# Optimization experiments

Measured on AMD Instinct MI355X. Metric: run time of the kernel, lower is better.

The kernel has to match this reference:

```python
import jax, jax.numpy as jnp
import numpy as np

D = 1024      # hidden_dim
H = 16        # num_heads
KV = 8        # num_kv_heads
HD = D // H   # head_size = 64
M = 3584      # intermediate_dim
E = 8         # num_local_experts
TOPK = 2      # num_experts_per_tok
EPS = 1e-6
ROPE_THETA = 10000.0


def setup_inputs() -> dict:
    key = jax.random.key(0)
    ks = jax.random.split(key, 12)
    s = 0.02
    B, S = 2, 1024
    return {
        "x": jax.random.normal(ks[0], (B, S, D), jnp.float32),
        "ln1_w": jnp.ones((D,), jnp.float32),
        "ln2_w": jnp.ones((D,), jnp.float32),
        "wq": jax.random.normal(ks[1], (D, H * HD), jnp.float32) * s,
        "wk": jax.random.normal(ks[2], (D, KV * HD), jnp.float32) * s,
        "wv": jax.random.normal(ks[3], (D, KV * HD), jnp.float32) * s,
        "wo": jax.random.normal(ks[4], (H * HD, D), jnp.float32) * s,
        "router_w": jax.random.normal(ks[5], (D, E), jnp.float32) * s,
        "w_gate": jax.random.normal(ks[6], (E, D, M), jnp.float32) * s,
        "w_up": jax.random.normal(ks[7], (E, D, M), jnp.float32) * s,
        "w_down": jax.random.normal(ks[8], (E, M, D), jnp.float32) * s,
    }


def _rmsnorm(x, w, eps=EPS):
    xf = x.astype(jnp.float32)
    var = jnp.mean(xf * xf, axis=-1, keepdims=True)
    return (xf * jax.lax.rsqrt(var + eps)).astype(x.dtype) * w


def _rope(q, k):
    # q: [B,S,H,HD], k: [B,S,KV,HD]
    S = q.shape[1]
    inv_freq = 1.0 / (ROPE_THETA ** (jnp.arange(0, HD, 2, dtype=jnp.float32) / HD))
    ang = jnp.arange(S, dtype=jnp.float32)[:, None] * inv_freq[None, :]  # [S, HD/2]
    cos = jnp.concatenate([jnp.cos(ang), jnp.cos(ang)], axis=-1)[None, :, None, :]
    sin = jnp.concatenate([jnp.sin(ang), jnp.sin(ang)], axis=-1)[None, :, None, :]

    def rot_half(t):
        t1, t2 = jnp.split(t, 2, axis=-1)
        return jnp.concatenate([-t2, t1], axis=-1)

    return q * cos + rot_half(q) * sin, k * cos + rot_half(k) * sin


def reference(x, ln1_w, ln2_w, wq, wk, wv, wo, router_w, w_gate, w_up, w_down):
    B, S, _ = x.shape

    # ---- self-attention block ----
    h = _rmsnorm(x, ln1_w)
    q = (h @ wq).reshape(B, S, H, HD)
    k = (h @ wk).reshape(B, S, KV, HD)
    v = (h @ wv).reshape(B, S, KV, HD)
    q, k = _rope(q, k)
    rep = H // KV
    k = jnp.repeat(k, rep, axis=2)  # [B,S,H,HD]
    v = jnp.repeat(v, rep, axis=2)
    scores = jnp.einsum("bqhd,bkhd->bhqk", q, k) / jnp.sqrt(jnp.float32(HD))
    causal = jnp.tril(jnp.ones((S, S), bool))
    scores = jnp.where(causal[None, None], scores, jnp.finfo(scores.dtype).min)
    attn = jax.nn.softmax(scores, axis=-1)
    ao = jnp.einsum("bhqk,bkhd->bqhd", attn, v).reshape(B, S, H * HD)
    x = x + ao @ wo

    # ---- sparse MoE block (top-2 routing, SwiGLU experts) ----
    h = _rmsnorm(x, ln2_w)
    logits = h @ router_w                       # [B,S,E]
    probs = jax.nn.softmax(logits, axis=-1)
    topv, topi = jax.lax.top_k(probs, TOPK)     # [B,S,K]
    topv = topv / jnp.sum(topv, axis=-1, keepdims=True)
    # dense combine weights [B,S,E]: zero for unselected experts
    weights = jnp.sum(jax.nn.one_hot(topi, E, dtype=h.dtype) * topv[..., None], axis=-2)
    gate = jnp.einsum("bsd,edm->bsem", h, w_gate)
    up = jnp.einsum("bsd,edm->bsem", h, w_up)
    act = jax.nn.silu(gate) * up * weights[..., None]
    moe = jnp.einsum("bsem,emd->bsd", act, w_down)
    return x + moe
```

## Files before the change

kernel.cpp:

```cpp
#include <hip/hip_runtime.h>

typedef __attribute__((ext_vector_type(8))) short short8;
typedef __attribute__((ext_vector_type(4))) float f32x4;
typedef unsigned int u32;

#define DI static __device__ __forceinline__

DI unsigned short f2bf(float f) {
  unsigned u = __builtin_bit_cast(unsigned, f);
  u += 0x7fffu + ((u >> 16) & 1u);
  return (unsigned short)(u >> 16);
}
DI float bf2f(unsigned short b) {
  unsigned u = ((unsigned)b) << 16;
  return __builtin_bit_cast(float, u);
}

DI void gload16(const unsigned short* g, unsigned short* l) {
  __builtin_amdgcn_global_load_lds(
      (const __attribute__((address_space(1))) u32*)g,
      (__attribute__((address_space(3))) u32*)l, 16, 0, 0);
}

static constexpr int NT   = 2048;
static constexpr int SEQ  = 1024;
static constexpr int DIM  = 1024;
static constexpr int NH   = 16;
static constexpr int NKV  = 8;
static constexpr int HD   = 64;
static constexpr int MDIM = 3584;
static constexpr int NE   = 8;
static constexpr int QW   = 2048;
static constexpr int GUW  = 2 * MDIM;

__global__ void __launch_bounds__(256) transpose_kernel(
    const float* __restrict__ in, unsigned short* __restrict__ out,
    int R, int C, size_t in_estride, size_t out_estride) {
  __shared__ unsigned short tl[64][66];
  int e = blockIdx.z;
  const float* ip = in + (size_t)e * in_estride;
  unsigned short* op = out + (size_t)e * out_estride;
  int c0 = blockIdx.x * 64, r0 = blockIdx.y * 64;
  int tid = threadIdx.x;
  {
    int lr = tid >> 4, lc = (tid & 15) * 4;
#pragma unroll
    for (int p = 0; p < 4; ++p) {
      int r = p * 16 + lr;
      float4 v = *(const float4*)(ip + (size_t)(r0 + r) * C + c0 + lc);
      tl[lc + 0][r] = f2bf(v.x);
      tl[lc + 1][r] = f2bf(v.y);
      tl[lc + 2][r] = f2bf(v.z);
      tl[lc + 3][r] = f2bf(v.w);
    }
  }
  __syncthreads();
  {
    int c = tid >> 2, rc = (tid & 3) * 16;
    unsigned short tmp[16];
#pragma unroll
    for (int j = 0; j < 8; ++j) {
      u32 w = *(const u32*)&tl[c][rc + j * 2];
      tmp[j * 2] = (unsigned short)w;
      tmp[j * 2 + 1] = (unsigned short)(w >> 16);
    }
    unsigned short* dst = op + (size_t)(c0 + c) * R + r0 + rc;
#pragma unroll
    for (int j = 0; j < 2; ++j)
      *(uint4*)(dst + j * 8) = *(const uint4*)&tmp[j * 8];
  }
}

__global__ void __launch_bounds__(256) rmsnorm_kernel(const float* __restrict__ x,
                                                      const float* __restrict__ w,
                                                      unsigned short* __restrict__ out) {
  int row = blockIdx.x;
  const float* xr = x + (size_t)row * DIM;
  int i = threadIdx.x * 4;
  float4 v = *(const float4*)(xr + i);
  float s = v.x * v.x + v.y * v.y + v.z * v.z + v.w * v.w;
  for (int o = 32; o; o >>= 1) s += __shfl_xor(s, o);
  __shared__ float red[4];
  if ((threadIdx.x & 63) == 0) red[threadIdx.x >> 6] = s;
  __syncthreads();
  s = red[0] + red[1] + red[2] + red[3];
  float r = rsqrtf(s * (1.0f / DIM) + 1e-6f);
  float4 wv = *(const float4*)(w + i);
  ushort4 o4;
  o4.x = f2bf(v.x * r * wv.x);
  o4.y = f2bf(v.y * r * wv.y);
  o4.z = f2bf(v.z * r * wv.z);
  o4.w = f2bf(v.w * r * wv.w);
  *(ushort4*)(out + (size_t)row * DIM + i) = o4;
}

template <int GATHER, int EPI, int NNT>
__global__ void __launch_bounds__(256) gemmT_kernel(
    const unsigned short* __restrict__ A, int lda,
    const unsigned short* __restrict__ B, int ldb, size_t b_estride,
    void* __restrict__ Cv, int ldc,
    const float* __restrict__ resid,
    int M, int K,
    const int* __restrict__ lists, const int* __restrict__ cnt,
    int ks_count, size_t ks_stride) {
  constexpr int BN = NNT * 32;
  constexpr int NBLK = BN / 64;
  int zz = blockIdx.z;
  int e = zz / ks_count, ks = zz - e * ks_count;
  int KL = K / ks_count;
  int kbase = ks * KL;

  int count = M;
  const int* lst = nullptr;
  if (GATHER != 0) {
    count = cnt[e];
    if (count <= 0) return;
    lst = lists + e * NT;
    B += b_estride * (size_t)e;
  }
  int m0 = blockIdx.y * 128;
  if (m0 >= count) return;
  int n0 = blockIdx.x * BN;

  __shared__ unsigned short sA[3][128 * 32];
  __shared__ unsigned short sB[3][BN * 32];

  int tid = threadIdx.x, w = tid >> 6, lane = tid & 63;
  int l15 = lane & 15, lhi = lane >> 4;

  int srow = w * 16 + (lane >> 2);
  int schunk = ((lane & 3) ^ ((lane >> 2) & 3)) * 8;
  const unsigned short *aSrc0, *aSrc1;
  const unsigned short* bSrc[NBLK];
  {
    int mr0 = m0 + srow, mr1 = m0 + 64 + srow;
    int ar0, ar1;
    if (GATHER == 0) { ar0 = mr0; ar1 = mr1; }
    else {
      int c0i = mr0 < count ? mr0 : count - 1;
      int c1i = mr1 < count ? mr1 : count - 1;
      int p0 = lst[c0i], p1 = lst[c1i];
      ar0 = (GATHER == 1) ? (p0 >> 1) : p0;
      ar1 = (GATHER == 1) ? (p1 >> 1) : p1;
    }
    aSrc0 = A + (size_t)ar0 * lda + kbase + schunk;
    aSrc1 = A + (size_t)ar1 * lda + kbase + schunk;
#pragma unroll
    for (int s = 0; s < NBLK; ++s)
      bSrc[s] = B + (size_t)(n0 + s * 64 + srow) * ldb + kbase + schunk;
  }
  unsigned ldst = (unsigned)(w * 16) * 32;

  auto stage = [&](int buf, int k0) {
    gload16(aSrc0 + k0, &sA[buf][ldst]);
    gload16(aSrc1 + k0, &sA[buf][ldst + 64 * 32]);
#pragma unroll
    for (int s = 0; s < NBLK; ++s)
      gload16(bSrc[s] + k0, &sB[buf][ldst + s * 64 * 32]);
  };

  f32x4 acc[4][NNT] = {};
  int wm = w >> 1, wn = w & 1;
  int aoff[4], boff[NNT];
#pragma unroll
  for (int t = 0; t < 4; ++t) {
    int row = wm * 64 + t * 16 + l15;
    aoff[t] = row * 32 + ((lhi ^ (row & 3)) * 8);
  }
#pragma unroll
  for (int t = 0; t < NNT; ++t) {
    int col = wn * (BN / 2) + t * 16 + l15;
    boff[t] = col * 32 + ((lhi ^ (col & 3)) * 8);
  }

  int nsteps = KL / 32;
  stage(0, 0);
  if (nsteps > 1) stage(1, 32);

  int cur = 0, stg = 2;
  for (int t = 0; t < nsteps; ++t) {
    if (t + 1 < nsteps) {
      if constexpr (NNT == 8) asm volatile("s_waitcnt vmcnt(6)" ::: "memory");
      else                    asm volatile("s_waitcnt vmcnt(4)" ::: "memory");
    } else {
      asm volatile("s_waitcnt vmcnt(0)" ::: "memory");
    }
    __builtin_amdgcn_s_barrier();
    __builtin_amdgcn_sched_barrier(0);
    if (t + 2 < nsteps) stage(stg, (t + 2) * 32);
    const unsigned short* pa = sA[cur];
    const unsigned short* pb = sB[cur];
    short8 af[4], bfr[NNT];
#pragma unroll
    for (int q = 0; q < 4; ++q) af[q] = *(const short8*)&pa[aoff[q]];
#pragma unroll
    for (int q = 0; q < NNT; ++q) bfr[q] = *(const short8*)&pb[boff[q]];
    __builtin_amdgcn_s_setprio(1);
#pragma unroll
    for (int mi = 0; mi < 4; ++mi)
#pragma unroll
      for (int ni = 0; ni < NNT; ++ni)
        acc[mi][ni] =
            __builtin_amdgcn_mfma_f32_16x16x32_bf16(af[mi], bfr[ni], acc[mi][ni], 0, 0, 0);
    __builtin_amdgcn_s_setprio(0);
    cur = (cur == 2) ? 0 : cur + 1;
    stg = (stg == 2) ? 0 : stg + 1;
  }

#pragma unroll
  for (int mi = 0; mi < 4; ++mi) {
#pragma unroll
    for (int r = 0; r < 4; ++r) {
      int mr = m0 + wm * 64 + mi * 16 + lhi * 4 + r;
      if (GATHER != 0 && mr >= count) continue;
      size_t crow = (GATHER != 0) ? (size_t)lst[mr] : (size_t)mr;
#pragma unroll
      for (int ni = 0; ni < NNT; ++ni) {
        int n = n0 + wn * (BN / 2) + ni * 16 + l15;
        float val = acc[mi][ni][r];
        if (EPI == 0)
          ((unsigned short*)Cv)[crow * ldc + n] = f2bf(val);
        else if (EPI == 1)
          ((float*)Cv)[crow * ldc + n] = val + resid[crow * ldc + n];
        else
          ((float*)Cv)[(size_t)ks * ks_stride + crow * ldc + n] = val;
      }
    }
  }
}

__global__ void __launch_bounds__(256) rope_kernel(unsigned short* __restrict__ qkv) {
  int g = blockIdx.x * 256 + threadIdx.x;
  int i = g & 31;
  int hh = (g >> 5) % (NH + NKV);
  int tok = g / (32 * (NH + NKV));
  if (tok >= NT) return;
  int s = tok & (SEQ - 1);
  float inv = exp2f((float)i * (-13.287712379549449f / 32.0f));
  float ang = (float)s * inv;
  float sn = sinf(ang);
  float c = cosf(ang);
  int col = (hh < NH) ? hh * HD : DIM + (hh - NH) * HD;
  unsigned short* ptr = qkv + (size_t)tok * QW + col;
  float a = bf2f(ptr[i]), b2 = bf2f(ptr[i + 32]);
  ptr[i] = f2bf(a * c - b2 * sn);
  ptr[i + 32] = f2bf(b2 * c + a * sn);
}

__global__ void __launch_bounds__(64) attn_kernel(const unsigned short* __restrict__ qkv,
                                                  unsigned short* __restrict__ ao) {
  __shared__ unsigned short Ps[16 * 64];
  int bid = blockIdx.x;
  int qt = bid & 63;
  int h = (bid >> 6) & 15;
  int b = bid >> 10;
  int lane = threadIdx.x, l15 = lane & 15, lhi = lane >> 4;
  int q0 = qt * 16, kvh = h >> 1;
  int kcol = DIM + kvh * HD, vcol = DIM + NKV * HD + kvh * HD;

  const unsigned short* qp = qkv + ((size_t)(b * SEQ + q0 + l15)) * QW + h * HD + lhi * 8;
  short8 aq0 = *(const short8*)qp;
  short8 aq1 = *(const short8*)(qp + 32);

  float m[4] = {-1e30f, -1e30f, -1e30f, -1e30f};
  float l[4] = {0.f, 0.f, 0.f, 0.f};
  f32x4 accO[4] = {};

  int nkb = (qt >> 2) + 1;
  for (int kb_ = 0; kb_ < nkb; ++kb_) {
    int kbase = kb_ * 64;
    f32x4 s[4];
#pragma unroll
    for (int ct = 0; ct < 4; ++ct) {
      const unsigned short* kp =
          qkv + ((size_t)(b * SEQ + kbase + ct * 16 + l15)) * QW + kcol + lhi * 8;
      short8 k0v = *(const short8*)kp;
      short8 k1v = *(const short8*)(kp + 32);
      f32x4 a = {};
      a = __builtin_amdgcn_mfma_f32_16x16x32_bf16(aq0, k0v, a, 0, 0, 0);
      a = __builtin_amdgcn_mfma_f32_16x16x32_bf16(aq1, k1v, a, 0, 0, 0);
      int kpos = kbase + ct * 16 + l15;
#pragma unroll
      for (int r = 0; r < 4; ++r) {
        float v = a[r] * 0.125f;
        if (kpos > q0 + lhi * 4 + r) v = -1e30f;
        s[ct][r] = v;
      }
    }
    float nm[4], al[4], rs[4];
#pragma unroll
    for (int r = 0; r < 4; ++r) {
      float mb = fmaxf(fmaxf(s[0][r], s[1][r]), fmaxf(s[2][r], s[3][r]));
      mb = fmaxf(mb, __shfl_xor(mb, 1));
      mb = fmaxf(mb, __shfl_xor(mb, 2));
      mb = fmaxf(mb, __shfl_xor(mb, 4));
      mb = fmaxf(mb, __shfl_xor(mb, 8));
      nm[r] = fmaxf(m[r], mb);
      al[r] = __expf(m[r] - nm[r]);
      m[r] = nm[r];
      rs[r] = 0.f;
    }
#pragma unroll
    for (int ct = 0; ct < 4; ++ct) {
#pragma unroll
      for (int r = 0; r < 4; ++r) {
        float p = __expf(s[ct][r] - nm[r]);
        rs[r] += p;
        int q = lhi * 4 + r;
        Ps[q * 64 + ((ct * 16 + l15) ^ (lhi << 4))] = f2bf(p);
      }
    }
#pragma unroll
    for (int r = 0; r < 4; ++r) {
      rs[r] += __shfl_xor(rs[r], 1);
      rs[r] += __shfl_xor(rs[r], 2);
      rs[r] += __shfl_xor(rs[r], 4);
      rs[r] += __shfl_xor(rs[r], 8);
      l[r] = l[r] * al[r] + rs[r];
    }
#pragma unroll
    for (int dt = 0; dt < 4; ++dt)
#pragma unroll
      for (int r = 0; r < 4; ++r) accO[dt][r] *= al[r];

    int pswz = (l15 >> 2) << 4;
    short8 ap0 = *(const short8*)&Ps[l15 * 64 + ((lhi * 8) ^ pswz)];
    short8 ap1 = *(const short8*)&Ps[l15 * 64 + ((32 + lhi * 8) ^ pswz)];
#pragma unroll
    for (int dt = 0; dt < 4; ++dt) {
#pragma unroll
      for (int ks = 0; ks < 2; ++ks) {
        const unsigned short* vp =
            qkv + ((size_t)(b * SEQ + kbase + ks * 32 + lhi * 8)) * QW + vcol + dt * 16 + l15;
        short8 vf;
#pragma unroll
        for (int j = 0; j < 8; ++j) vf[j] = (short)vp[(size_t)j * QW];
        accO[dt] = __builtin_amdgcn_mfma_f32_16x16x32_bf16(ks ? ap1 : ap0, vf, accO[dt], 0, 0, 0);
      }
    }
  }
  float invl[4];
#pragma unroll
  for (int r = 0; r < 4; ++r) invl[r] = 1.f / l[r];
#pragma unroll
  for (int dt = 0; dt < 4; ++dt)
#pragma unroll
    for (int r = 0; r < 4; ++r)
      ao[((size_t)(b * SEQ + q0 + lhi * 4 + r)) * DIM + h * HD + dt * 16 + l15] =
          f2bf(accO[dt][r] * invl[r]);
}

__global__ void zero_cnt_kernel(int* __restrict__ cnt) {
  if (threadIdx.x < NE) cnt[threadIdx.x] = 0;
}

__global__ void __launch_bounds__(64) router_kernel(const float* __restrict__ x2,
                                                    const float* __restrict__ ln2w,
                                                    const float* __restrict__ rw,
                                                    float* __restrict__ wts,
                                                    int* __restrict__ cnt,
                                                    int* __restrict__ lists) {
  int t = blockIdx.x, lane = threadIdx.x;
  const float* xr = x2 + (size_t)t * DIM;
  float xs[16];
  double ssq = 0.0;
#pragma unroll
  for (int j = 0; j < 16; ++j) {
    xs[j] = xr[lane + j * 64];
    ssq += (double)xs[j] * xs[j];
  }
  for (int o = 32; o; o >>= 1) ssq += __shfl_xor(ssq, o);
  double r = rsqrt(ssq * (1.0 / DIM) + 1e-6);
  double p[NE] = {};
#pragma unroll
  for (int j = 0; j < 16; ++j) {
    int i = lane + j * 64;
    double hv = (double)xs[j] * r * (double)ln2w[i];
    const float* rwp = rw + (size_t)i * NE;
#pragma unroll
    for (int e = 0; e < NE; ++e) p[e] += hv * (double)rwp[e];
  }
  for (int o = 32; o; o >>= 1) {
#pragma unroll
    for (int e = 0; e < NE; ++e) p[e] += __shfl_xor(p[e], o);
  }
  if (lane == 0) {
    int i1 = 0;
    for (int e = 1; e < NE; ++e)
      if (p[e] > p[i1]) i1 = e;
    int i2 = (i1 == 0) ? 1 : 0;
    for (int e = 0; e < NE; ++e)
      if (e != i1 && p[e] > p[i2]) i2 = e;
    double mx = fmax(p[i1], p[i2]);
    double e1 = exp(p[i1] - mx), e2 = exp(p[i2] - mx);
    double inv = 1.0 / (e1 + e2);
    wts[t * 2] = (float)(e1 * inv);
    wts[t * 2 + 1] = (float)(e2 * inv);
    int pos1 = atomicAdd(&cnt[i1], 1);
    lists[i1 * NT + pos1] = t * 2;
    int pos2 = atomicAdd(&cnt[i2], 1);
    lists[i2 * NT + pos2] = t * 2 + 1;
  }
}

__global__ void __launch_bounds__(256) swiglu_kernel(const unsigned short* __restrict__ gu,
                                                     const float* __restrict__ wts,
                                                     unsigned short* __restrict__ act) {
  size_t i = ((size_t)blockIdx.x * 256 + threadIdx.x) * 8;
  int pid = (int)(i / MDIM);
  int mcol = (int)(i - (size_t)pid * MDIM);
  float w = wts[pid];
  const unsigned short* row = gu + (size_t)pid * GUW;
  short8 g8 = *(const short8*)(row + mcol);
  short8 u8 = *(const short8*)(row + MDIM + mcol);
  short8 o8;
#pragma unroll
  for (int j = 0; j < 8; ++j) {
    float gv = bf2f((unsigned short)g8[j]);
    float uv = bf2f((unsigned short)u8[j]);
    float sv = gv / (1.f + __expf(-gv));
    o8[j] = (short)f2bf(sv * uv * w);
  }
  *(short8*)(act + i) = o8;
}

__global__ void __launch_bounds__(256) combine_kernel(const float* __restrict__ x2,
                                                      const float* __restrict__ part,
                                                      float* __restrict__ out) {
  const size_t KSS = (size_t)2 * NT * DIM;
  size_t idx = ((size_t)blockIdx.x * 256 + threadIdx.x) * 4;
  size_t t = idx >> 10;
  size_t d = idx & 1023;
  float4 a = *(const float4*)(x2 + idx);
  float4 b0 = *(const float4*)(part + (t * 2) * DIM + d);
  float4 c0 = *(const float4*)(part + (t * 2 + 1) * DIM + d);
  float4 b1 = *(const float4*)(part + KSS + (t * 2) * DIM + d);
  float4 c1 = *(const float4*)(part + KSS + (t * 2 + 1) * DIM + d);
  float4 o;
  o.x = a.x + b0.x + c0.x + b1.x + c1.x;
  o.y = a.y + b0.y + c0.y + b1.y + c1.y;
  o.z = a.z + b0.z + c0.z + b1.z + c1.z;
  o.w = a.w + b0.w + c0.w + b1.w + c1.w;
  *(float4*)(out + idx) = o;
}

extern "C" void kernel_launch(void* const* d_in, const int* in_sizes, int n_in,
                              void* d_out, int out_size, void* d_ws, size_t ws_size,
                              hipStream_t stream) {
  const float* x   = (const float*)d_in[0];
  const float* ln1 = (const float*)d_in[1];
  const float* ln2 = (const float*)d_in[2];
  const float* wq  = (const float*)d_in[3];
  const float* wk  = (const float*)d_in[4];
  const float* wv  = (const float*)d_in[5];
  const float* wo  = (const float*)d_in[6];
  const float* rw  = (const float*)d_in[7];
  const float* wg  = (const float*)d_in[8];
  const float* wu  = (const float*)d_in[9];
  const float* wd  = (const float*)d_in[10];
  float* out = (float*)d_out;

  char* p = (char*)d_ws;
  auto take = [&](size_t bytes) {
    char* q = p;
    p += (bytes + 255) & ~(size_t)255;
    return q;
  };
  unsigned short* wguT = (unsigned short*)take((size_t)NE * GUW * DIM * 2);
  unsigned short* wdT  = (unsigned short*)take((size_t)NE * DIM * MDIM * 2);
  float*          x2   = (float*)take((size_t)NT * DIM * 4);
  unsigned short* h2   = (unsigned short*)take((size_t)NT * DIM * 2);
  float*          part = (float*)take((size_t)2 * 2 * NT * DIM * 4);
  unsigned short* act  = (unsigned short*)take((size_t)2 * NT * MDIM * 2);
  float*          wtsb = (float*)take((size_t)2 * NT * 4);
  int*            cntb = (int*)take(NE * 4);
  int*            listsb = (int*)take((size_t)NE * NT * 4);
  char* X = p;
  unsigned short* wqkvT = (unsigned short*)X;
  unsigned short* woT   = wqkvT + (size_t)QW * DIM;
  unsigned short* h1    = woT + (size_t)DIM * DIM;
  unsigned short* qkv   = h1 + (size_t)NT * DIM;
  unsigned short* aob   = qkv + (size_t)NT * QW;
  unsigned short* gu    = (unsigned short*)X;

  transpose_kernel<<<dim3(16, 16, 1), 256, 0, stream>>>(wq, wqkvT, DIM, DIM, 0, 0);
  transpose_kernel<<<dim3(8, 16, 1), 256, 0, stream>>>(wk, wqkvT + (size_t)DIM * DIM, DIM, 512, 0, 0);
  transpose_kernel<<<dim3(8, 16, 1), 256, 0, stream>>>(wv, wqkvT + (size_t)(DIM + 512) * DIM, DIM, 512, 0, 0);
  transpose_kernel<<<dim3(16, 16, 1), 256, 0, stream>>>(wo, woT, DIM, DIM, 0, 0);
  transpose_kernel<<<dim3(56, 16, NE), 256, 0, stream>>>(
      wg, wguT, DIM, MDIM, (size_t)DIM * MDIM, (size_t)GUW * DIM);
  transpose_kernel<<<dim3(56, 16, NE), 256, 0, stream>>>(
      wu, wguT + (size_t)MDIM * DIM, DIM, MDIM, (size_t)DIM * MDIM, (size_t)GUW * DIM);
  transpose_kernel<<<dim3(16, 56, NE), 256, 0, stream>>>(
      wd, wdT, MDIM, DIM, (size_t)MDIM * DIM, (size_t)DIM * MDIM);

  rmsnorm_kernel<<<NT, 256, 0, stream>>>(x, ln1, h1);
  gemmT_kernel<0, 0, 4><<<dim3(QW / 128, NT / 128, 1), 256, 0, stream>>>(
      h1, DIM, wqkvT, DIM, 0, qkv, QW, nullptr, NT, DIM, nullptr, nullptr, 1, 0);
  rope_kernel<<<(NT * (NH + NKV) * 32) / 256, 256, 0, stream>>>(qkv);
  attn_kernel<<<NT * NH / 16, 64, 0, stream>>>(qkv, aob);
  gemmT_kernel<0, 1, 4><<<dim3(DIM / 128, NT / 128, 1), 256, 0, stream>>>(
      aob, DIM, woT, DIM, 0, x2, DIM, x, NT, DIM, nullptr, nullptr, 1, 0);

  rmsnorm_kernel<<<NT, 256, 0, stream>>>(x2, ln2, h2);
  zero_cnt_kernel<<<1, 64, 0, stream>>>(cntb);
  router_kernel<<<NT, 64, 0, stream>>>(x2, ln2, rw, wtsb, cntb, listsb);

  gemmT_kernel<1, 0, 8><<<dim3(GUW / 256, 16, NE), 256, 0, stream>>>(
      h2, DIM, wguT, DIM, (size_t)GUW * DIM, gu, GUW, nullptr, 0, DIM, listsb, cntb, 1, 0);
  swiglu_kernel<<<(int)(((size_t)2 * NT * MDIM) / (256 * 8)), 256, 0, stream>>>(
      gu, wtsb, act);
  gemmT_kernel<2, 2, 4><<<dim3(DIM / 128, 16, NE * 2), 256, 0, stream>>>(
      act, MDIM, wdT, MDIM, (size_t)DIM * MDIM, part, DIM, nullptr, 0, MDIM, listsb, cntb,
      2, (size_t)2 * NT * DIM);

  combine_kernel<<<(NT * DIM) / 1024, 256, 0, stream>>>(x2, part, out);
}
```

Measured before the change: 586.4 us.

## Fuse SwiGLU into gate/up GEMM, transpose V, change LDS swizzle, split-K 4

```diff
diff --git a/kernel.cpp b/kernel.cpp
--- a/kernel.cpp
+++ b/kernel.cpp
@@ -33,6 +33,7 @@
 static constexpr int QW   = 2048;
 static constexpr int GUW  = 2 * MDIM;
 
+template <int ROWMAP>
 __global__ void __launch_bounds__(256) transpose_kernel(
     const float* __restrict__ in, unsigned short* __restrict__ out,
     int R, int C, size_t in_estride, size_t out_estride) {
@@ -64,10 +65,43 @@
       tmp[j * 2] = (unsigned short)w;
       tmp[j * 2 + 1] = (unsigned short)(w >> 16);
     }
-    unsigned short* dst = op + (size_t)(c0 + c) * R + r0 + rc;
+    int cg = c0 + c;
+    int orow;
+    if (ROWMAP == 0) orow = cg;
+    else orow = ((cg >> 4) << 5) + (cg & 15) + (ROWMAP == 2 ? 16 : 0);
+    unsigned short* dst = op + (size_t)orow * R + r0 + rc;
 #pragma unroll
     for (int j = 0; j < 2; ++j)
       *(uint4*)(dst + j * 8) = *(const uint4*)&tmp[j * 8];
+  }
+}
+
+__global__ void __launch_bounds__(256) vtrans_kernel(const unsigned short* __restrict__ qkv,
+                                                     unsigned short* __restrict__ vT) {
+  __shared__ unsigned short tl[64][66];
+  int s0 = blockIdx.x * 64;
+  int kvh = blockIdx.y;
+  int b = blockIdx.z;
+  int tid = threadIdx.x;
+  {
+    int r = tid >> 2, cc = (tid & 3) * 16;
+    const unsigned short* src =
+        qkv + ((size_t)(b * SEQ + s0 + r)) * QW + (DIM + NKV * HD + kvh * HD) + cc;
+    unsigned short tmp[16];
+    *(uint4*)&tmp[0] = *(const uint4*)src;
+    *(uint4*)&tmp[8] = *(const uint4*)(src + 8);
+#pragma unroll
+    for (int j = 0; j < 16; ++j) tl[cc + j][r] = tmp[j];
+  }
+  __syncthreads();
+  {
+    int h = tid >> 2, sc = (tid & 3) * 16;
+    unsigned short o[16];
+#pragma unroll
+    for (int j = 0; j < 16; ++j) o[j] = tl[h][sc + j];
+    unsigned short* dst = vT + (((size_t)(b * NKV + kvh) * HD + h) * SEQ) + s0 + sc;
+    *(uint4*)dst = *(const uint4*)&o[0];
+    *(uint4*)(dst + 8) = *(const uint4*)&o[8];
   }
 }
 
@@ -129,7 +163,7 @@
   int l15 = lane & 15, lhi = lane >> 4;
 
   int srow = w * 16 + (lane >> 2);
-  int schunk = ((lane & 3) ^ ((lane >> 2) & 3)) * 8;
+  int schunk = (((lane & 3) - ((lane >> 3) & 3)) & 3) * 8;
   const unsigned short *aSrc0, *aSrc1;
   const unsigned short* bSrc[NBLK];
   {
@@ -161,16 +195,17 @@
 
   f32x4 acc[4][NNT] = {};
   int wm = w >> 1, wn = w & 1;
+  int fslot = ((lhi + (l15 >> 1)) & 3) * 8;
   int aoff[4], boff[NNT];
 #pragma unroll
   for (int t = 0; t < 4; ++t) {
     int row = wm * 64 + t * 16 + l15;
-    aoff[t] = row * 32 + ((lhi ^ (row & 3)) * 8);
+    aoff[t] = row * 32 + fslot;
   }
 #pragma unroll
   for (int t = 0; t < NNT; ++t) {
     int col = wn * (BN / 2) + t * 16 + l15;
-    boff[t] = col * 32 + ((lhi ^ (col & 3)) * 8);
+    boff[t] = col * 32 + fslot;
   }
 
   int nsteps = KL / 32;
@@ -214,16 +249,28 @@
       int mr = m0 + wm * 64 + mi * 16 + lhi * 4 + r;
       if (GATHER != 0 && mr >= count) continue;
       size_t crow = (GATHER != 0) ? (size_t)lst[mr] : (size_t)mr;
-#pragma unroll
-      for (int ni = 0; ni < NNT; ++ni) {
-        int n = n0 + wn * (BN / 2) + ni * 16 + l15;
-        float val = acc[mi][ni][r];
-        if (EPI == 0)
-          ((unsigned short*)Cv)[crow * ldc + n] = f2bf(val);
-        else if (EPI == 1)
-          ((float*)Cv)[crow * ldc + n] = val + resid[crow * ldc + n];
-        else
-          ((float*)Cv)[(size_t)ks * ks_stride + crow * ldc + n] = val;
+      if (EPI == 3) {
+        float wgt = resid[crow];
+        int colbase = (n0 + wn * (BN / 2)) >> 1;
+#pragma unroll
+        for (int ni = 0; ni < NNT; ni += 2) {
+          float g = acc[mi][ni][r], u = acc[mi][ni + 1][r];
+          float sv = g / (1.f + __expf(-g));
+          ((unsigned short*)Cv)[crow * ldc + colbase + (ni >> 1) * 16 + l15] =
+              f2bf(sv * u * wgt);
+        }
+      } else {
+#pragma unroll
+        for (int ni = 0; ni < NNT; ++ni) {
+          int n = n0 + wn * (BN / 2) + ni * 16 + l15;
+          float val = acc[mi][ni][r];
+          if (EPI == 0)
+            ((unsigned short*)Cv)[crow * ldc + n] = f2bf(val);
+          else if (EPI == 1)
+            ((float*)Cv)[crow * ldc + n] = val + resid[crow * ldc + n];
+          else
+            ((float*)Cv)[(size_t)ks * ks_stride + crow * ldc + n] = val;
+        }
       }
     }
   }
@@ -248,6 +295,7 @@
 }
 
 __global__ void __launch_bounds__(64) attn_kernel(const unsigned short* __restrict__ qkv,
+                                                  const unsigned short* __restrict__ vT,
                                                   unsigned short* __restrict__ ao) {
   __shared__ unsigned short Ps[16 * 64];
   int bid = blockIdx.x;
@@ -256,11 +304,13 @@
   int b = bid >> 10;
   int lane = threadIdx.x, l15 = lane & 15, lhi = lane >> 4;
   int q0 = qt * 16, kvh = h >> 1;
-  int kcol = DIM + kvh * HD, vcol = DIM + NKV * HD + kvh * HD;
+  int kcol = DIM + kvh * HD;
 
   const unsigned short* qp = qkv + ((size_t)(b * SEQ + q0 + l15)) * QW + h * HD + lhi * 8;
   short8 aq0 = *(const short8*)qp;
   short8 aq1 = *(const short8*)(qp + 32);
+
+  const unsigned short* vbase = vT + ((size_t)(b * NKV + kvh) * HD) * SEQ;
 
   float m[4] = {-1e30f, -1e30f, -1e30f, -1e30f};
   float l[4] = {0.f, 0.f, 0.f, 0.f};
@@ -331,10 +381,8 @@
 #pragma unroll
       for (int ks = 0; ks < 2; ++ks) {
         const unsigned short* vp =
-            qkv + ((size_t)(b * SEQ + kbase + ks * 32 + lhi * 8)) * QW + vcol + dt * 16 + l15;
-        short8 vf;
-#pragma unroll
-        for (int j = 0; j < 8; ++j) vf[j] = (short)vp[(size_t)j * QW];
+            vbase + ((size_t)(dt * 16 + l15)) * SEQ + kbase + ks * 32 + lhi * 8;
+        short8 vf = *(const short8*)vp;
         accO[dt] = __builtin_amdgcn_mfma_f32_16x16x32_bf16(ks ? ap1 : ap0, vf, accO[dt], 0, 0, 0);
       }
     }
@@ -403,27 +451,6 @@
   }
 }
 
-__global__ void __launch_bounds__(256) swiglu_kernel(const unsigned short* __restrict__ gu,
-                                                     const float* __restrict__ wts,
-                                                     unsigned short* __restrict__ act) {
-  size_t i = ((size_t)blockIdx.x * 256 + threadIdx.x) * 8;
-  int pid = (int)(i / MDIM);
-  int mcol = (int)(i - (size_t)pid * MDIM);
-  float w = wts[pid];
-  const unsigned short* row = gu + (size_t)pid * GUW;
-  short8 g8 = *(const short8*)(row + mcol);
-  short8 u8 = *(const short8*)(row + MDIM + mcol);
-  short8 o8;
-#pragma unroll
-  for (int j = 0; j < 8; ++j) {
-    float gv = bf2f((unsigned short)g8[j]);
-    float uv = bf2f((unsigned short)u8[j]);
-    float sv = gv / (1.f + __expf(-gv));
-    o8[j] = (short)f2bf(sv * uv * w);
-  }
-  *(short8*)(act + i) = o8;
-}
-
 __global__ void __launch_bounds__(256) combine_kernel(const float* __restrict__ x2,
                                                       const float* __restrict__ part,
                                                       float* __restrict__ out) {
@@ -431,16 +458,16 @@
   size_t idx = ((size_t)blockIdx.x * 256 + threadIdx.x) * 4;
   size_t t = idx >> 10;
   size_t d = idx & 1023;
-  float4 a = *(const float4*)(x2 + idx);
-  float4 b0 = *(const float4*)(part + (t * 2) * DIM + d);
-  float4 c0 = *(const float4*)(part + (t * 2 + 1) * DIM + d);
-  float4 b1 = *(const float4*)(part + KSS + (t * 2) * DIM + d);
-  float4 c1 = *(const float4*)(part + KSS + (t * 2 + 1) * DIM + d);
-  float4 o;
-  o.x = a.x + b0.x + c0.x + b1.x + c1.x;
-  o.y = a.y + b0.y + c0.y + b1.y + c1.y;
-  o.z = a.z + b0.z + c0.z + b1.z + c1.z;
-  o.w = a.w + b0.w + c0.w + b1.w + c1.w;
+  float4 o = *(const float4*)(x2 + idx);
+#pragma unroll
+  for (int s = 0; s < 4; ++s) {
+    float4 b0 = *(const float4*)(part + s * KSS + (t * 2) * DIM + d);
+    float4 c0 = *(const float4*)(part + s * KSS + (t * 2 + 1) * DIM + d);
+    o.x += b0.x + c0.x;
+    o.y += b0.y + c0.y;
+    o.z += b0.z + c0.z;
+    o.w += b0.w + c0.w;
+  }
   *(float4*)(out + idx) = o;
 }
 
@@ -470,7 +497,7 @@
   unsigned short* wdT  = (unsigned short*)take((size_t)NE * DIM * MDIM * 2);
   float*          x2   = (float*)take((size_t)NT * DIM * 4);
   unsigned short* h2   = (unsigned short*)take((size_t)NT * DIM * 2);
-  float*          part = (float*)take((size_t)2 * 2 * NT * DIM * 4);
+  float*          part = (float*)take((size_t)4 * 2 * NT * DIM * 4);
   unsigned short* act  = (unsigned short*)take((size_t)2 * NT * MDIM * 2);
   float*          wtsb = (float*)take((size_t)2 * NT * 4);
   int*            cntb = (int*)take(NE * 4);
@@ -481,24 +508,25 @@
   unsigned short* h1    = woT + (size_t)DIM * DIM;
   unsigned short* qkv   = h1 + (size_t)NT * DIM;
   unsigned short* aob   = qkv + (size_t)NT * QW;
-  unsigned short* gu    = (unsigned short*)X;
-
-  transpose_kernel<<<dim3(16, 16, 1), 256, 0, stream>>>(wq, wqkvT, DIM, DIM, 0, 0);
-  transpose_kernel<<<dim3(8, 16, 1), 256, 0, stream>>>(wk, wqkvT + (size_t)DIM * DIM, DIM, 512, 0, 0);
-  transpose_kernel<<<dim3(8, 16, 1), 256, 0, stream>>>(wv, wqkvT + (size_t)(DIM + 512) * DIM, DIM, 512, 0, 0);
-  transpose_kernel<<<dim3(16, 16, 1), 256, 0, stream>>>(wo, woT, DIM, DIM, 0, 0);
-  transpose_kernel<<<dim3(56, 16, NE), 256, 0, stream>>>(
+  unsigned short* vT    = aob + (size_t)NT * DIM;
+
+  transpose_kernel<0><<<dim3(16, 16, 1), 256, 0, stream>>>(wq, wqkvT, DIM, DIM, 0, 0);
+  transpose_kernel<0><<<dim3(8, 16, 1), 256, 0, stream>>>(wk, wqkvT + (size_t)DIM * DIM, DIM, 512, 0, 0);
+  transpose_kernel<0><<<dim3(8, 16, 1), 256, 0, stream>>>(wv, wqkvT + (size_t)(DIM + 512) * DIM, DIM, 512, 0, 0);
+  transpose_kernel<0><<<dim3(16, 16, 1), 256, 0, stream>>>(wo, woT, DIM, DIM, 0, 0);
+  transpose_kernel<1><<<dim3(56, 16, NE), 256, 0, stream>>>(
       wg, wguT, DIM, MDIM, (size_t)DIM * MDIM, (size_t)GUW * DIM);
-  transpose_kernel<<<dim3(56, 16, NE), 256, 0, stream>>>(
-      wu, wguT + (size_t)MDIM * DIM, DIM, MDIM, (size_t)DIM * MDIM, (size_t)GUW * DIM);
-  transpose_kernel<<<dim3(16, 56, NE), 256, 0, stream>>>(
+  transpose_kernel<2><<<dim3(56, 16, NE), 256, 0, stream>>>(
+      wu, wguT, DIM, MDIM, (size_t)DIM * MDIM, (size_t)GUW * DIM);
+  transpose_kernel<0><<<dim3(16, 56, NE), 256, 0, stream>>>(
       wd, wdT, MDIM, DIM, (size_t)MDIM * DIM, (size_t)DIM * MDIM);
 
   rmsnorm_kernel<<<NT, 256, 0, stream>>>(x, ln1, h1);
   gemmT_kernel<0, 0, 4><<<dim3(QW / 128, NT / 128, 1), 256, 0, stream>>>(
       h1, DIM, wqkvT, DIM, 0, qkv, QW, nullptr, NT, DIM, nullptr, nullptr, 1, 0);
   rope_kernel<<<(NT * (NH + NKV) * 32) / 256, 256, 0, stream>>>(qkv);
-  attn_kernel<<<NT * NH / 16, 64, 0, stream>>>(qkv, aob);
+  vtrans_kernel<<<dim3(SEQ / 64, NKV, 2), 256, 0, stream>>>(qkv, vT);
+  attn_kernel<<<NT * NH / 16, 64, 0, stream>>>(qkv, vT, aob);
   gemmT_kernel<0, 1, 4><<<dim3(DIM / 128, NT / 128, 1), 256, 0, stream>>>(
       aob, DIM, woT, DIM, 0, x2, DIM, x, NT, DIM, nullptr, nullptr, 1, 0);
 
@@ -506,13 +534,11 @@
   zero_cnt_kernel<<<1, 64, 0, stream>>>(cntb);
   router_kernel<<<NT, 64, 0, stream>>>(x2, ln2, rw, wtsb, cntb, listsb);
 
-  gemmT_kernel<1, 0, 8><<<dim3(GUW / 256, 16, NE), 256, 0, stream>>>(
-      h2, DIM, wguT, DIM, (size_t)GUW * DIM, gu, GUW, nullptr, 0, DIM, listsb, cntb, 1, 0);
-  swiglu_kernel<<<(int)(((size_t)2 * NT * MDIM) / (256 * 8)), 256, 0, stream>>>(
-      gu, wtsb, act);
-  gemmT_kernel<2, 2, 4><<<dim3(DIM / 128, 16, NE * 2), 256, 0, stream>>>(
+  gemmT_kernel<1, 3, 4><<<dim3(GUW / 128, 16, NE), 256, 0, stream>>>(
+      h2, DIM, wguT, DIM, (size_t)GUW * DIM, act, MDIM, wtsb, 0, DIM, listsb, cntb, 1, 0);
+  gemmT_kernel<2, 2, 4><<<dim3(DIM / 128, 16, NE * 4), 256, 0, stream>>>(
       act, MDIM, wdT, MDIM, (size_t)DIM * MDIM, part, DIM, nullptr, 0, MDIM, listsb, cntb,
-      2, (size_t)2 * NT * DIM);
+      4, (size_t)2 * NT * DIM);
 
   combine_kernel<<<(NT * DIM) / 1024, 256, 0, stream>>>(x2, part, out);
 }
```

New measurement: 507.8 us. 1.15x faster.
